# Optimization experiments

Measured on AMD Instinct MI355X. Metric: run time of the kernel, lower is better.

The kernel has to match this reference:

```python
import jax, jax.numpy as jnp
import numpy as np

GRID_SIZE = 3
SPLINE_ORDER = 3
N_BASIS = GRID_SIZE + SPLINE_ORDER  # 6


def make_grid(in_features, dtype=jnp.float32):
    # efficient-kan grid buffer: extended uniform knots over grid_range=[-1, 1]
    h = 2.0 / GRID_SIZE
    g = jnp.arange(-SPLINE_ORDER, GRID_SIZE + SPLINE_ORDER + 1, dtype=dtype) * h - 1.0
    return jnp.tile(g[None, :], (in_features, 1))  # (in, G + 2S + 1)


def b_splines(x, grid):
    # x: (N, in), grid: (in, G+2S+1) -> (N, in, G+S) via Cox-de Boor recursion
    xb = x[..., None]
    bases = ((xb >= grid[:, :-1]) & (xb < grid[:, 1:])).astype(x.dtype)
    for k in range(1, SPLINE_ORDER + 1):
        bases = ((xb - grid[:, : -(k + 1)]) / (grid[:, k:-1] - grid[:, : -(k + 1)]) * bases[..., :-1]
                 + (grid[:, k + 1:] - xb) / (grid[:, k + 1:] - grid[:, 1:-k]) * bases[..., 1:])
    return bases


def kan_linear(x, base_w, spline_w, scaler, grid):
    # base path: silu(x) @ W_base^T ; spline path: contraction of basis with scaled spline weights
    base = jax.nn.silu(x) @ base_w.T
    scaled_sw = spline_w * scaler[..., None]  # (out, in, K)
    spl = jnp.einsum('nik,oik->no', b_splines(x, grid), scaled_sw)
    return base + spl


def setup_inputs() -> dict:
    key = jax.random.key(0)
    ks = jax.random.split(key, 7)
    B, C, P, D, H = 8, 8, 128, 256, 1024
    s = 0.05
    return {
        'x': jax.random.normal(ks[0], (B, C, P, D), dtype=jnp.float32),
        'base_w1': s * jax.random.normal(ks[1], (H, D), dtype=jnp.float32),
        'spline_w1': s * jax.random.normal(ks[2], (H, D, N_BASIS), dtype=jnp.float32),
        'scaler1': 1.0 + s * jax.random.normal(ks[3], (H, D), dtype=jnp.float32),
        'base_w2': s * jax.random.normal(ks[4], (D, H), dtype=jnp.float32),
        'spline_w2': s * jax.random.normal(ks[5], (D, H, N_BASIS), dtype=jnp.float32),
        'scaler2': 1.0 + s * jax.random.normal(ks[6], (D, H), dtype=jnp.float32),
    }


def reference(x, base_w1, spline_w1, scaler1, base_w2, spline_w2, scaler2):
    B, C, P, D = x.shape
    H = base_w1.shape[0]
    xf = x.reshape(-1, D)  # KANLinear flattens leading dims to tokens
    g1 = make_grid(D, x.dtype)
    g2 = make_grid(H, x.dtype)
    h = kan_linear(xf, base_w1, spline_w1, scaler1, g1)
    h = jax.nn.gelu(h, approximate=False)  # torch F.gelu default = exact erf
    # dropout is identity in eval / with p used as inference baseline
    y = kan_linear(h, base_w2, spline_w2, scaler2, g2)
    return y.reshape(B, C, P, D)
```

## Files before the change

### kernel.cpp

```cpp
#include <hip/hip_runtime.h>
#include <hip/hip_bf16.h>
#include <math.h>


typedef __attribute__((ext_vector_type(8))) short bf16x8;
typedef __attribute__((ext_vector_type(4))) float f32x4;
typedef __attribute__((ext_vector_type(4))) unsigned short u16x4;

#define TOKENS 8192
#define D_IN   256
#define D_HID  1024

__device__ __forceinline__ void kan_features(float x, float f[8]) {
    f[0] = x * __builtin_amdgcn_rcpf(1.0f + __expf(-x));
    const float s = (x + 1.0f) * 1.5f + 3.0f;
    const float cf = floorf(s);
    const float u = s - cf;
    const int c = (int)cf;
    const float u2 = u * u, u3 = u2 * u;
    const float k6 = 1.0f / 6.0f;
    const float v3 = u3 * k6;
    const float v2 = (-3.0f * u3 + 3.0f * u2 + 3.0f * u + 1.0f) * k6;
    const float v1 = (3.0f * u3 - 6.0f * u2 + 4.0f) * k6;
    const float w1 = 1.0f - u;
    const float v0 = w1 * w1 * w1 * k6;
    const bool in = (s >= 0.0f) && (s < 9.0f);
#pragma unroll
    for (int j = 0; j < 6; ++j) {
        int d = c - j;
        float bv = (d == 0) ? v3 : (d == 1) ? v2 : (d == 2) ? v1 : (d == 3) ? v0 : 0.0f;
        f[1 + j] = in ? bv : 0.0f;
    }
    f[7] = 0.0f;
}

__device__ __forceinline__ void features_to_bf16(const float f[8], __hip_bfloat16 fb[8]) {
#pragma unroll
    for (int j = 0; j < 8; ++j) fb[j] = __float2bfloat16(f[j]);
}

__global__ void init_fused(const float* __restrict__ X, __hip_bfloat16* __restrict__ F,
                           const float* __restrict__ bw1, const float* __restrict__ sw1,
                           const float* __restrict__ sc1, __hip_bfloat16* __restrict__ W1,
                           const float* __restrict__ bw2, const float* __restrict__ sw2,
                           const float* __restrict__ sc2, __hip_bfloat16* __restrict__ W2) {
    const int b = blockIdx.x;
    if (b < 8192) {
        int idx = b * 256 + threadIdx.x;
        float f[8];
        kan_features(X[idx], f);
        __hip_bfloat16 fb[8];
        features_to_bf16(f, fb);
        *(bf16x8*)&F[(size_t)idx * 8] = *(bf16x8*)fb;
        return;
    }
    const bool w1 = (b < 9216);
    int idx = (w1 ? (b - 8192) : (b - 9216)) * 256 + threadIdx.x;
    const float* bw = w1 ? bw1 : bw2;
    const float* sw = w1 ? sw1 : sw2;
    const float* sc = w1 ? sc1 : sc2;
    __hip_bfloat16* Wo = w1 ? W1 : W2;
    float scl = sc[idx];
    __hip_bfloat16 row[8];
    row[0] = __float2bfloat16(bw[idx]);
#pragma unroll
    for (int j = 0; j < 6; ++j)
        row[1 + j] = __float2bfloat16(sw[idx * 6 + j] * scl);
    row[7] = __float2bfloat16(0.0f);
    *(bf16x8*)&Wo[(size_t)idx * 8] = *(bf16x8*)row;
}

#define GLL(src, dst) __builtin_amdgcn_global_load_lds(                         \
    (const __attribute__((address_space(1))) void*)(src),                       \
    (__attribute__((address_space(3))) void*)(dst), 16, 0, 0)

__global__ __launch_bounds__(512, 2)
void kan_gemm1(const __hip_bfloat16* __restrict__ A,
               const __hip_bfloat16* __restrict__ W,
               __hip_bfloat16* __restrict__ H) {
    constexpr int K = D_IN * 8;
    constexpr int NT = K / 64;
    __shared__ __hip_bfloat16 Al[2][128 * 64];
    __shared__ __hip_bfloat16 Bl[2][128 * 64];

    const int tid = threadIdx.x;
    const int wid = tid >> 6, lane = tid & 63;
    const int wm = wid >> 2, wn = wid & 3;
    const int lr = lane & 15, lg = lane >> 4;
    const int n0 = blockIdx.x * 128, o0 = blockIdx.y * 128;

    int srow[2], sslot[2];
#pragma unroll
    for (int p = 0; p < 2; ++p) {
        int item = tid + p * 512;
        srow[p] = item >> 3;
        sslot[p] = (item & 7) ^ (srow[p] & 7);
    }
    int aoff[2][4], boff[2][2];
#pragma unroll
    for (int ks = 0; ks < 2; ++ks) {
#pragma unroll
        for (int f = 0; f < 4; ++f) {
            int ar = wm * 64 + f * 16 + lr;
            aoff[ks][f] = ar * 64 + (((ks * 4 + lg) ^ (ar & 7)) * 8);
        }
#pragma unroll
        for (int f = 0; f < 2; ++f) {
            int br = wn * 32 + f * 16 + lr;
            boff[ks][f] = br * 64 + (((ks * 4 + lg) ^ (br & 7)) * 8);
        }
    }

    f32x4 acc[4][2] = {};

#define STG1(buf, kt)                                                           \
    do {                                                                        \
        _Pragma("unroll")                                                       \
        for (int p = 0; p < 2; ++p) {                                           \
            GLL(A + (size_t)(n0 + srow[p]) * K + (kt) * 64 + sslot[p] * 8,      \
                &Al[buf][(tid + p * 512) * 8]);                                 \
            GLL(W + (size_t)(o0 + srow[p]) * K + (kt) * 64 + sslot[p] * 8,      \
                &Bl[buf][(tid + p * 512) * 8]);                                 \
        }                                                                       \
    } while (0)

    STG1(0, 0);
    STG1(1, 1);
    for (int t = 0; t < NT; ++t) {
        const int cur = t & 1;
        asm volatile("s_waitcnt vmcnt(4)" ::: "memory");
        __builtin_amdgcn_s_barrier();
        __builtin_amdgcn_sched_barrier(0);
        __builtin_amdgcn_s_setprio(1);
#pragma unroll
        for (int ks = 0; ks < 2; ++ks) {
            bf16x8 af[4], bfr[2];
#pragma unroll
            for (int f = 0; f < 4; ++f) af[f] = *(const bf16x8*)&Al[cur][aoff[ks][f]];
#pragma unroll
            for (int f = 0; f < 2; ++f) bfr[f] = *(const bf16x8*)&Bl[cur][boff[ks][f]];
#pragma unroll
            for (int fm = 0; fm < 4; ++fm)
#pragma unroll
                for (int fn = 0; fn < 2; ++fn)
                    acc[fm][fn] = __builtin_amdgcn_mfma_f32_16x16x32_bf16(
                        af[fm], bfr[fn], acc[fm][fn], 0, 0, 0);
        }
        __builtin_amdgcn_s_setprio(0);
        asm volatile("s_waitcnt lgkmcnt(0)" ::: "memory");
        __builtin_amdgcn_s_barrier();
        __builtin_amdgcn_sched_barrier(0);
        const int kn = (t + 2 < NT) ? t + 2 : NT - 1;
        STG1(cur, kn);
    }
#undef STG1
#pragma unroll
    for (int fm = 0; fm < 4; ++fm) {
#pragma unroll
        for (int fn = 0; fn < 2; ++fn) {
            int col = o0 + wn * 32 + fn * 16 + lr;
#pragma unroll
            for (int r = 0; r < 4; ++r) {
                int row = n0 + wm * 64 + fm * 16 + lg * 4 + r;
                float v = acc[fm][fn][r];
                float g = 0.5f * v * (1.0f + erff(v * 0.70710678118f));
                H[(size_t)row * D_HID + col] = __float2bfloat16(g);
            }
        }
    }
}

__global__ __launch_bounds__(512, 2)
void kan_gemm2(const __hip_bfloat16* __restrict__ H,
               const __hip_bfloat16* __restrict__ W,
               __hip_bfloat16* __restrict__ P) {
    constexpr int OUT = D_IN, KD = D_HID * 8;
    constexpr int NTT = KD / 64;
    __shared__ __hip_bfloat16 Al[128 * 64];
    __shared__ __hip_bfloat16 Bl[256 * 64];

    const int tid = threadIdx.x;
    const int wid = tid >> 6, lane = tid & 63;
    const int wm = wid >> 2, wn = wid & 3;
    const int lr = lane & 15, lg = lane >> 4;
    const int n0 = blockIdx.x * 128;

    const int per = NTT / 8;
    const int ks0 = blockIdx.z * per, ks1 = ks0 + per;

    int srow[4], sslot[4];
#pragma unroll
    for (int p = 0; p < 4; ++p) {
        int item = tid + p * 512;
        srow[p] = item >> 3;
        sslot[p] = (item & 7) ^ (srow[p] & 7);
    }
    const int ar0 = tid >> 3, ac = tid & 7;
    const __hip_bfloat16* hp0 = H + (size_t)(n0 + ar0) * D_HID + ac;
    const __hip_bfloat16* hp1 = H + (size_t)(n0 + ar0 + 64) * D_HID + ac;
    const int aw0 = ar0 * 64 + ((ac ^ (ar0 & 7)) * 8);
    const int aw1 = (ar0 + 64) * 64 + ((ac ^ (ar0 & 7)) * 8);

    int aoff[2][4], boff[2][4];
#pragma unroll
    for (int ks = 0; ks < 2; ++ks)
#pragma unroll
        for (int f = 0; f < 4; ++f) {
            int ar = wm * 64 + f * 16 + lr;
            int br = wn * 64 + f * 16 + lr;
            aoff[ks][f] = ar * 64 + (((ks * 4 + lg) ^ (ar & 7)) * 8);
            boff[ks][f] = br * 64 + (((ks * 4 + lg) ^ (br & 7)) * 8);
        }

    f32x4 acc[4][4] = {};

    float hv0 = __bfloat162float(hp0[(size_t)ks0 * 8]);
    float hv1 = __bfloat162float(hp1[(size_t)ks0 * 8]);

    for (int kt = ks0; kt < ks1; ++kt) {
        float hc0 = hv0, hc1 = hv1;
        const int knext = (kt + 1 < ks1) ? kt + 1 : ks1 - 1;
        hv0 = __bfloat162float(hp0[(size_t)knext * 8]);
        hv1 = __bfloat162float(hp1[(size_t)knext * 8]);
        {
            float ff[8]; __hip_bfloat16 fb[8];
            kan_features(hc0, ff); features_to_bf16(ff, fb);
            *(bf16x8*)&Al[aw0] = *(bf16x8*)fb;
            kan_features(hc1, ff); features_to_bf16(ff, fb);
            *(bf16x8*)&Al[aw1] = *(bf16x8*)fb;
        }
#pragma unroll
        for (int p = 0; p < 4; ++p)
            GLL(W + (size_t)srow[p] * KD + (size_t)kt * 64 + sslot[p] * 8,
                &Bl[(tid + p * 512) * 8]);
        __syncthreads();
#pragma unroll
        for (int ks = 0; ks < 2; ++ks) {
            bf16x8 af[4], bfr[4];
#pragma unroll
            for (int f = 0; f < 4; ++f) af[f] = *(const bf16x8*)&Al[aoff[ks][f]];
#pragma unroll
            for (int f = 0; f < 4; ++f) bfr[f] = *(const bf16x8*)&Bl[boff[ks][f]];
#pragma unroll
            for (int fm = 0; fm < 4; ++fm)
#pragma unroll
                for (int fn = 0; fn < 4; ++fn)
                    acc[fm][fn] = __builtin_amdgcn_mfma_f32_16x16x32_bf16(
                        af[fm], bfr[fn], acc[fm][fn], 0, 0, 0);
        }
        __syncthreads();
    }

    float* Pl = (float*)Bl;
    const size_t zoff = (size_t)blockIdx.z * TOKENS * OUT;
#pragma unroll
    for (int q = 0; q < 4; ++q) {
        __syncthreads();
        if (wm == (q >> 1)) {
#pragma unroll
            for (int fp = 0; fp < 2; ++fp) {
                int fm = (q & 1) * 2 + fp;
#pragma unroll
                for (int fn = 0; fn < 4; ++fn) {
                    int c = wn * 64 + fn * 16 + lr;
#pragma unroll
                    for (int r = 0; r < 4; ++r)
                        Pl[(fp * 16 + lg * 4 + r) * 256 + c] = acc[fm][fn][r];
                }
            }
        }
        __syncthreads();
#pragma unroll
        for (int p = 0; p < 4; ++p) {
            int v = tid + p * 512;
            int row = v >> 6, cv = (v & 63) * 4;
            const float* src = &Pl[row * 256 + cv];
            __hip_bfloat16 ob[4];
#pragma unroll
            for (int j = 0; j < 4; ++j) ob[j] = __float2bfloat16(src[j]);
            *(u16x4*)&P[zoff + (size_t)(n0 + q * 32 + row) * OUT + cv] =
                *(const u16x4*)ob;
        }
    }
}

__global__ void reduce_split(const __hip_bfloat16* __restrict__ P,
                             float* __restrict__ out, int nvec) {
    int i = blockIdx.x * 256 + threadIdx.x;
    if (i >= nvec) return;
    float s[4] = {0.f, 0.f, 0.f, 0.f};
#pragma unroll
    for (int z = 0; z < 8; ++z) {
        u16x4 v = *(const u16x4*)&P[(size_t)z * TOKENS * D_IN + (size_t)i * 4];
#pragma unroll
        for (int j = 0; j < 4; ++j) {
            unsigned int bits = ((unsigned int)(unsigned short)v[j]) << 16;
            s[j] += __uint_as_float(bits);
        }
    }
    f32x4 o = {s[0], s[1], s[2], s[3]};
    *(f32x4*)&out[(size_t)i * 4] = o;
}

extern "C" void kernel_launch(void* const* d_in, const int* in_sizes, int n_in,
                              void* d_out, int out_size, void* d_ws, size_t ws_size,
                              hipStream_t stream) {
    const float* x   = (const float*)d_in[0];
    const float* bw1 = (const float*)d_in[1];
    const float* sw1 = (const float*)d_in[2];
    const float* sc1 = (const float*)d_in[3];
    const float* bw2 = (const float*)d_in[4];
    const float* sw2 = (const float*)d_in[5];
    const float* sc2 = (const float*)d_in[6];
    float* out = (float*)d_out;

    char* ws = (char*)d_ws;
    __hip_bfloat16* W1 = (__hip_bfloat16*)ws;
    __hip_bfloat16* W2 = (__hip_bfloat16*)(ws + (4ull << 20));
    __hip_bfloat16* F1 = (__hip_bfloat16*)(ws + (8ull << 20));
    __hip_bfloat16* Hb = (__hip_bfloat16*)(ws + (40ull << 20));
    __hip_bfloat16* Pp = (__hip_bfloat16*)(ws + (72ull << 20));

    if (ws_size < (104ull << 20)) return;

    init_fused<<<10240, 256, 0, stream>>>(x, F1, bw1, sw1, sc1, W1, bw2, sw2, sc2, W2);

    kan_gemm1<<<dim3(TOKENS / 128, D_HID / 128), 512, 0, stream>>>(F1, W1, Hb);

    kan_gemm2<<<dim3(TOKENS / 128, 1, 8), 512, 0, stream>>>(Hb, W2, Pp);

    const int nvec = TOKENS * D_IN / 4;
    reduce_split<<<(nvec + 255) / 256, 256, 0, stream>>>(Pp, out, nvec);
}
```

Measured before the change: 127.4 us.

## Register-prefetch weight tiles two steps ahead instead of direct global-to-LDS loads

Replaces the per-iteration global-to-LDS weight loads with register prefetching of the next two k-tiles using a double register buffer, storing them to LDS at the start of each tile. Hidden-activation loads are prefetched the same way. Explicit s_waitcnt, sched barriers and raw s_barrier calls replace __syncthreads to control scheduling, so global latency can overlap with MFMA work. This raises register pressure, which can lower occupancy. The loop also assumes an even tile count and does an extra VGPR-to-LDS copy.

```diff
diff --git a/kernel.cpp b/kernel.cpp
--- a/kernel.cpp
+++ b/kernel.cpp
@@ -214,42 +214,67 @@
 
     f32x4 acc[4][4] = {};
 
-    float hv0 = __bfloat162float(hp0[(size_t)ks0 * 8]);
-    float hv1 = __bfloat162float(hp1[(size_t)ks0 * 8]);
-
-    for (int kt = ks0; kt < ks1; ++kt) {
-        float hc0 = hv0, hc1 = hv1;
-        const int knext = (kt + 1 < ks1) ? kt + 1 : ks1 - 1;
-        hv0 = __bfloat162float(hp0[(size_t)knext * 8]);
-        hv1 = __bfloat162float(hp1[(size_t)knext * 8]);
-        {
-            float ff[8]; __hip_bfloat16 fb[8];
-            kan_features(hc0, ff); features_to_bf16(ff, fb);
-            *(bf16x8*)&Al[aw0] = *(bf16x8*)fb;
-            kan_features(hc1, ff); features_to_bf16(ff, fb);
-            *(bf16x8*)&Al[aw1] = *(bf16x8*)fb;
-        }
-#pragma unroll
-        for (int p = 0; p < 4; ++p)
-            GLL(W + (size_t)srow[p] * KD + (size_t)kt * 64 + sslot[p] * 8,
-                &Bl[(tid + p * 512) * 8]);
-        __syncthreads();
-#pragma unroll
-        for (int ks = 0; ks < 2; ++ks) {
-            bf16x8 af[4], bfr[4];
-#pragma unroll
-            for (int f = 0; f < 4; ++f) af[f] = *(const bf16x8*)&Al[aoff[ks][f]];
-#pragma unroll
-            for (int f = 0; f < 4; ++f) bfr[f] = *(const bf16x8*)&Bl[boff[ks][f]];
-#pragma unroll
-            for (int fm = 0; fm < 4; ++fm)
-#pragma unroll
-                for (int fn = 0; fn < 4; ++fn)
-                    acc[fm][fn] = __builtin_amdgcn_mfma_f32_16x16x32_bf16(
-                        af[fm], bfr[fn], acc[fm][fn], 0, 0, 0);
-        }
-        __syncthreads();
-    }
+#define LOADB(br, kt)                                                           \
+    do {                                                                        \
+        _Pragma("unroll")                                                       \
+        for (int p = 0; p < 4; ++p)                                             \
+            br[p] = *(const bf16x8*)&W[(size_t)srow[p] * KD + (size_t)(kt) * 64 \
+                                        + sslot[p] * 8];                        \
+    } while (0)
+
+#define TILE2(T, br, h0, h1, DO)                                                \
+    do {                                                                        \
+        _Pragma("unroll")                                                       \
+        for (int p = 0; p < 4; ++p)                                             \
+            *(bf16x8*)&Bl[(tid + p * 512) * 8] = br[p];                         \
+        {                                                                       \
+            float ff[8]; __hip_bfloat16 fb[8];                                  \
+            kan_features(__bfloat162float(h0), ff); features_to_bf16(ff, fb);   \
+            *(bf16x8*)&Al[aw0] = *(bf16x8*)fb;                                  \
+            kan_features(__bfloat162float(h1), ff); features_to_bf16(ff, fb);   \
+            *(bf16x8*)&Al[aw1] = *(bf16x8*)fb;                                  \
+        }                                                                       \
+        if (DO) {                                                               \
+            const int kn = ((T) + 2 < ks1) ? (T) + 2 : ks1 - 1;                 \
+            LOADB(br, kn);                                                      \
+            h0 = hp0[(size_t)kn * 8];                                           \
+            h1 = hp1[(size_t)kn * 8];                                           \
+        }                                                                       \
+        asm volatile("s_waitcnt lgkmcnt(0)" ::: "memory");                      \
+        __builtin_amdgcn_sched_barrier(0);                                      \
+        __builtin_amdgcn_s_barrier();                                           \
+        _Pragma("unroll")                                                       \
+        for (int ks = 0; ks < 2; ++ks) {                                        \
+            bf16x8 af[4], bfr[4];                                               \
+            _Pragma("unroll")                                                   \
+            for (int f = 0; f < 4; ++f) af[f] = *(const bf16x8*)&Al[aoff[ks][f]]; \
+            _Pragma("unroll")                                                   \
+            for (int f = 0; f < 4; ++f) bfr[f] = *(const bf16x8*)&Bl[boff[ks][f]]; \
+            _Pragma("unroll")                                                   \
+            for (int fm = 0; fm < 4; ++fm)                                      \
+                _Pragma("unroll")                                               \
+                for (int fn = 0; fn < 4; ++fn)                                  \
+                    acc[fm][fn] = __builtin_amdgcn_mfma_f32_16x16x32_bf16(      \
+                        af[fm], bfr[fn], acc[fm][fn], 0, 0, 0);                 \
+        }                                                                       \
+        asm volatile("" ::: "memory");                                          \
+        __builtin_amdgcn_s_barrier();                                           \
+        __builtin_amdgcn_sched_barrier(0);                                      \
+    } while (0)
+
+    bf16x8 brA[4], brB[4];
+    __hip_bfloat16 hA0, hA1, hB0, hB1;
+    LOADB(brA, ks0);
+    hA0 = hp0[(size_t)ks0 * 8];  hA1 = hp1[(size_t)ks0 * 8];
+    LOADB(brB, ks0 + 1);
+    hB0 = hp0[(size_t)(ks0 + 1) * 8];  hB1 = hp1[(size_t)(ks0 + 1) * 8];
+
+    for (int t = ks0; t < ks1; t += 2) {
+        TILE2(t,     brA, hA0, hA1, 1);
+        TILE2(t + 1, brB, hB0, hB1, (t + 2 < ks1));
+    }
+#undef TILE2
+#undef LOADB
 
     float* Pl = (float*)Bl;
     const size_t zoff = (size_t)blockIdx.z * TOKENS * OUT;
```

Result: slower. 154.4 us (+21.2%).

## Double threads per block in both GEMMs, halving per-wave M tile

Applied to the files above, without the earlier changes.

Both GEMM kernels now launch 1024 threads (16 waves) per block instead of 512, and each wave covers a 32-row slice of the 128-row tile instead of 64 rows, so it holds half as many accumulators. Staging loads per thread drop accordingly, and in gemm2 each thread computes KAN features for one hidden value instead of two. The goal is more waves to hide LDS and global latency. The cost is more barrier participants and lower MFMA work per LDS fragment load, since the B fragments are now reused across fewer M rows.

```diff
diff --git a/kernel.cpp b/kernel.cpp
--- a/kernel.cpp
+++ b/kernel.cpp
@@ -74,7 +74,7 @@
     (const __attribute__((address_space(1))) void*)(src),                       \
     (__attribute__((address_space(3))) void*)(dst), 16, 0, 0)
 
-__global__ __launch_bounds__(512, 2)
+__global__ __launch_bounds__(1024, 2)
 void kan_gemm1(const __hip_bfloat16* __restrict__ A,
                const __hip_bfloat16* __restrict__ W,
                __hip_bfloat16* __restrict__ H) {
@@ -89,58 +89,48 @@
     const int lr = lane & 15, lg = lane >> 4;
     const int n0 = blockIdx.x * 128, o0 = blockIdx.y * 128;
 
-    int srow[2], sslot[2];
-#pragma unroll
-    for (int p = 0; p < 2; ++p) {
-        int item = tid + p * 512;
-        srow[p] = item >> 3;
-        sslot[p] = (item & 7) ^ (srow[p] & 7);
-    }
-    int aoff[2][4], boff[2][2];
+    const int srow = tid >> 3;
+    const int sslot = (tid & 7) ^ (srow & 7);
+
+    int aoff[2][2], boff[2][2];
 #pragma unroll
     for (int ks = 0; ks < 2; ++ks) {
 #pragma unroll
-        for (int f = 0; f < 4; ++f) {
-            int ar = wm * 64 + f * 16 + lr;
+        for (int f = 0; f < 2; ++f) {
+            int ar = wm * 32 + f * 16 + lr;
             aoff[ks][f] = ar * 64 + (((ks * 4 + lg) ^ (ar & 7)) * 8);
-        }
-#pragma unroll
-        for (int f = 0; f < 2; ++f) {
             int br = wn * 32 + f * 16 + lr;
             boff[ks][f] = br * 64 + (((ks * 4 + lg) ^ (br & 7)) * 8);
         }
     }
 
-    f32x4 acc[4][2] = {};
+    f32x4 acc[2][2] = {};
 
 #define STG1(buf, kt)                                                           \
     do {                                                                        \
-        _Pragma("unroll")                                                       \
-        for (int p = 0; p < 2; ++p) {                                           \
-            GLL(A + (size_t)(n0 + srow[p]) * K + (kt) * 64 + sslot[p] * 8,      \
-                &Al[buf][(tid + p * 512) * 8]);                                 \
-            GLL(W + (size_t)(o0 + srow[p]) * K + (kt) * 64 + sslot[p] * 8,      \
-                &Bl[buf][(tid + p * 512) * 8]);                                 \
-        }                                                                       \
+        GLL(A + (size_t)(n0 + srow) * K + (kt) * 64 + sslot * 8,                \
+            &Al[buf][tid * 8]);                                                 \
+        GLL(W + (size_t)(o0 + srow) * K + (kt) * 64 + sslot * 8,                \
+            &Bl[buf][tid * 8]);                                                 \
     } while (0)
 
     STG1(0, 0);
     STG1(1, 1);
     for (int t = 0; t < NT; ++t) {
         const int cur = t & 1;
-        asm volatile("s_waitcnt vmcnt(4)" ::: "memory");
+        asm volatile("s_waitcnt vmcnt(2)" ::: "memory");
         __builtin_amdgcn_s_barrier();
         __builtin_amdgcn_sched_barrier(0);
         __builtin_amdgcn_s_setprio(1);
 #pragma unroll
         for (int ks = 0; ks < 2; ++ks) {
-            bf16x8 af[4], bfr[2];
-#pragma unroll
-            for (int f = 0; f < 4; ++f) af[f] = *(const bf16x8*)&Al[cur][aoff[ks][f]];
+            bf16x8 af[2], bfr[2];
+#pragma unroll
+            for (int f = 0; f < 2; ++f) af[f] = *(const bf16x8*)&Al[cur][aoff[ks][f]];
 #pragma unroll
             for (int f = 0; f < 2; ++f) bfr[f] = *(const bf16x8*)&Bl[cur][boff[ks][f]];
 #pragma unroll
-            for (int fm = 0; fm < 4; ++fm)
+            for (int fm = 0; fm < 2; ++fm)
 #pragma unroll
                 for (int fn = 0; fn < 2; ++fn)
                     acc[fm][fn] = __builtin_amdgcn_mfma_f32_16x16x32_bf16(
@@ -155,13 +145,13 @@
     }
 #undef STG1
 #pragma unroll
-    for (int fm = 0; fm < 4; ++fm) {
+    for (int fm = 0; fm < 2; ++fm) {
 #pragma unroll
         for (int fn = 0; fn < 2; ++fn) {
             int col = o0 + wn * 32 + fn * 16 + lr;
 #pragma unroll
             for (int r = 0; r < 4; ++r) {
-                int row = n0 + wm * 64 + fm * 16 + lg * 4 + r;
+                int row = n0 + wm * 32 + fm * 16 + lg * 4 + r;
                 float v = acc[fm][fn][r];
                 float g = 0.5f * v * (1.0f + erff(v * 0.70710678118f));
                 H[(size_t)row * D_HID + col] = __float2bfloat16(g);
@@ -170,7 +160,7 @@
     }
 }
 
-__global__ __launch_bounds__(512, 2)
+__global__ __launch_bounds__(1024, 2)
 void kan_gemm2(const __hip_bfloat16* __restrict__ H,
                const __hip_bfloat16* __restrict__ W,
                __hip_bfloat16* __restrict__ P) {
@@ -188,61 +178,59 @@
     const int per = NTT / 8;
     const int ks0 = blockIdx.z * per, ks1 = ks0 + per;
 
-    int srow[4], sslot[4];
-#pragma unroll
-    for (int p = 0; p < 4; ++p) {
-        int item = tid + p * 512;
+    int srow[2], sslot[2];
+#pragma unroll
+    for (int p = 0; p < 2; ++p) {
+        int item = tid + p * 1024;
         srow[p] = item >> 3;
         sslot[p] = (item & 7) ^ (srow[p] & 7);
     }
     const int ar0 = tid >> 3, ac = tid & 7;
     const __hip_bfloat16* hp0 = H + (size_t)(n0 + ar0) * D_HID + ac;
-    const __hip_bfloat16* hp1 = H + (size_t)(n0 + ar0 + 64) * D_HID + ac;
     const int aw0 = ar0 * 64 + ((ac ^ (ar0 & 7)) * 8);
-    const int aw1 = (ar0 + 64) * 64 + ((ac ^ (ar0 & 7)) * 8);
-
-    int aoff[2][4], boff[2][4];
-#pragma unroll
-    for (int ks = 0; ks < 2; ++ks)
+
+    int aoff[2][2], boff[2][4];
+#pragma unroll
+    for (int ks = 0; ks < 2; ++ks) {
+#pragma unroll
+        for (int f = 0; f < 2; ++f) {
+            int ar = wm * 32 + f * 16 + lr;
+            aoff[ks][f] = ar * 64 + (((ks * 4 + lg) ^ (ar & 7)) * 8);
+        }
 #pragma unroll
         for (int f = 0; f < 4; ++f) {
-            int ar = wm * 64 + f * 16 + lr;
             int br = wn * 64 + f * 16 + lr;
-            aoff[ks][f] = ar * 64 + (((ks * 4 + lg) ^ (ar & 7)) * 8);
             boff[ks][f] = br * 64 + (((ks * 4 + lg) ^ (br & 7)) * 8);
         }
-
-    f32x4 acc[4][4] = {};
+    }
+
+    f32x4 acc[2][4] = {};
 
     float hv0 = __bfloat162float(hp0[(size_t)ks0 * 8]);
-    float hv1 = __bfloat162float(hp1[(size_t)ks0 * 8]);
 
     for (int kt = ks0; kt < ks1; ++kt) {
-        float hc0 = hv0, hc1 = hv1;
+        float hc0 = hv0;
         const int knext = (kt + 1 < ks1) ? kt + 1 : ks1 - 1;
         hv0 = __bfloat162float(hp0[(size_t)knext * 8]);
-        hv1 = __bfloat162float(hp1[(size_t)knext * 8]);
         {
             float ff[8]; __hip_bfloat16 fb[8];
             kan_features(hc0, ff); features_to_bf16(ff, fb);
             *(bf16x8*)&Al[aw0] = *(bf16x8*)fb;
-            kan_features(hc1, ff); features_to_bf16(ff, fb);
-            *(bf16x8*)&Al[aw1] = *(bf16x8*)fb;
-        }
-#pragma unroll
-        for (int p = 0; p < 4; ++p)
+        }
+#pragma unroll
+        for (int p = 0; p < 2; ++p)
             GLL(W + (size_t)srow[p] * KD + (size_t)kt * 64 + sslot[p] * 8,
-                &Bl[(tid + p * 512) * 8]);
+                &Bl[(tid + p * 1024) * 8]);
         __syncthreads();
 #pragma unroll
         for (int ks = 0; ks < 2; ++ks) {
-            bf16x8 af[4], bfr[4];
-#pragma unroll
-            for (int f = 0; f < 4; ++f) af[f] = *(const bf16x8*)&Al[aoff[ks][f]];
+            bf16x8 af[2], bfr[4];
+#pragma unroll
+            for (int f = 0; f < 2; ++f) af[f] = *(const bf16x8*)&Al[aoff[ks][f]];
 #pragma unroll
             for (int f = 0; f < 4; ++f) bfr[f] = *(const bf16x8*)&Bl[boff[ks][f]];
 #pragma unroll
-            for (int fm = 0; fm < 4; ++fm)
+            for (int fm = 0; fm < 2; ++fm)
 #pragma unroll
                 for (int fn = 0; fn < 4; ++fn)
                     acc[fm][fn] = __builtin_amdgcn_mfma_f32_16x16x32_bf16(
@@ -256,23 +244,21 @@
 #pragma unroll
     for (int q = 0; q < 4; ++q) {
         __syncthreads();
-        if (wm == (q >> 1)) {
-#pragma unroll
-            for (int fp = 0; fp < 2; ++fp) {
-                int fm = (q & 1) * 2 + fp;
+        if (wm == q) {
+#pragma unroll
+            for (int fm = 0; fm < 2; ++fm)
 #pragma unroll
                 for (int fn = 0; fn < 4; ++fn) {
                     int c = wn * 64 + fn * 16 + lr;
 #pragma unroll
                     for (int r = 0; r < 4; ++r)
-                        Pl[(fp * 16 + lg * 4 + r) * 256 + c] = acc[fm][fn][r];
+                        Pl[(fm * 16 + lg * 4 + r) * 256 + c] = acc[fm][fn][r];
                 }
-            }
         }
         __syncthreads();
 #pragma unroll
-        for (int p = 0; p < 4; ++p) {
-            int v = tid + p * 512;
+        for (int p = 0; p < 2; ++p) {
+            int v = tid + p * 1024;
             int row = v >> 6, cv = (v & 63) * 4;
             const float* src = &Pl[row * 256 + cv];
             __hip_bfloat16 ob[4];
@@ -325,9 +311,9 @@
 
     init_fused<<<10240, 256, 0, stream>>>(x, F1, bw1, sw1, sc1, W1, bw2, sw2, sc2, W2);
 
-    kan_gemm1<<<dim3(TOKENS / 128, D_HID / 128), 512, 0, stream>>>(F1, W1, Hb);
-
-    kan_gemm2<<<dim3(TOKENS / 128, 1, 8), 512, 0, stream>>>(Hb, W2, Pp);
+    kan_gemm1<<<dim3(TOKENS / 128, D_HID / 128), 1024, 0, stream>>>(F1, W1, Hb);
+
+    kan_gemm2<<<dim3(TOKENS / 128, 1, 8), 1024, 0, stream>>>(Hb, W2, Pp);
 
     const int nvec = TOKENS * D_IN / 4;
     reduce_split<<<(nvec + 255) / 256, 256, 0, stream>>>(Pp, out, nvec);
```

After: 142.5 us. +11.9%, slower.
